# Optimization experiments

Measured on AMD Instinct MI355X. Metric: run time of the kernel, lower is better.

## Reference

```python
import jax, jax.numpy as jnp
import numpy as np

B, D_IN, D_COMMON = 16384, 2048, 1024
HIDDEN, D_OUT = 4096, 1024
N_EXPERTS = 4


def setup_inputs() -> dict:
    key = jax.random.key(0)
    ks = jax.random.split(key, 12)
    s = 0.02
    return {
        "x": jax.random.normal(ks[0], (B, D_IN), dtype=jnp.float32),
        "k": jax.random.randint(ks[1], (B,), 0, N_EXPERTS, dtype=jnp.int32),
        # per-key alignment Linear(D_IN -> D_COMMON), stored [in, out]
        "W_exp": jax.random.normal(ks[2], (N_EXPERTS, D_IN, D_COMMON), dtype=jnp.float32) * s,
        "b_exp": jax.random.normal(ks[3], (N_EXPERTS, D_COMMON), dtype=jnp.float32) * s,
        # dense MLP: common -> 4096 -> 4096 -> 1024
        "W1": jax.random.normal(ks[4], (D_COMMON, HIDDEN), dtype=jnp.float32) * s,
        "b1": jax.random.normal(ks[5], (HIDDEN,), dtype=jnp.float32) * s,
        "W2": jax.random.normal(ks[6], (HIDDEN, HIDDEN), dtype=jnp.float32) * s,
        "b2": jax.random.normal(ks[7], (HIDDEN,), dtype=jnp.float32) * s,
        "W3": jax.random.normal(ks[8], (HIDDEN, D_OUT), dtype=jnp.float32) * s,
        "b3": jax.random.normal(ks[9], (D_OUT,), dtype=jnp.float32) * s,
    }


def reference(x, k, W_exp, b_exp, W1, b1, W2, b2, W3, b3):
    # Key-routed per-row Linear: row i goes through expert k[i].
    # Compute all expert projections, then select per-row (vectorized dispatch).
    xW = jnp.einsum('bd,edc->ebc', x, W_exp)              # [E, B, common]
    onehot = jax.nn.one_hot(k, N_EXPERTS, dtype=x.dtype)  # [B, E]
    aligned = jnp.einsum('be,ebc->bc', onehot, xW) + b_exp[k]  # [B, common]
    # dense MLP with ReLU activations
    h = jax.nn.relu(aligned @ W1 + b1)
    h = jax.nn.relu(h @ W2 + b2)
    return h @ W3 + b3
```

## Files before the change

kernel.cpp:

```cpp
#include <hip/hip_runtime.h>
#include <stdint.h>

#define DEV static __device__ __forceinline__

typedef unsigned short u16;
typedef float  f32x4 __attribute__((ext_vector_type(4)));
typedef short  s16x8 __attribute__((ext_vector_type(8)));
typedef u16    u16x4 __attribute__((ext_vector_type(4)));

#define VMCNT(n) asm volatile("s_waitcnt vmcnt(" #n ")" ::: "memory")
#define BAR() __builtin_amdgcn_s_barrier()

DEV u16 f2bf(float f) {
  uint32_t u = __float_as_uint(f);
  u += 0x7FFFu + ((u >> 16) & 1u);
  return (u16)(u >> 16);
}

DEV void async16(const void* g, void* l) {
  __builtin_amdgcn_global_load_lds(
      (const __attribute__((address_space(1))) void*)g,
      (__attribute__((address_space(3))) void*)l, 16, 0, 0);
}

__global__ void route_zero(int* c) {
  if (threadIdx.x < 8) c[threadIdx.x] = 0;
}
__global__ void route_count(const int* __restrict__ k, int* __restrict__ c, int B) {
  int i = blockIdx.x * blockDim.x + threadIdx.x;
  if (i < B) atomicAdd(&c[k[i]], 1);
}
__global__ void route_scan(int* c) {
  if (threadIdx.x == 0) {
    int s = 0;
    for (int e = 0; e < 4; ++e) { c[8 + e] = s; s += c[e]; }
  }
}
__global__ void route_scatter(const int* __restrict__ k, int* __restrict__ c,
                              int* __restrict__ perm, int B) {
  int i = blockIdx.x * blockDim.x + threadIdx.x;
  if (i < B) {
    int e = k[i];
    int pos = atomicAdd(&c[4 + e], 1);
    perm[c[8 + e] + pos] = i;
  }
}

__global__ void cvt_f32_bf16(const float* __restrict__ src, u16* __restrict__ dst, long n4) {
  long i = (long)blockIdx.x * blockDim.x + threadIdx.x;
  long stride = (long)gridDim.x * blockDim.x;
  for (; i < n4; i += stride) {
    f32x4 v = ((const f32x4*)src)[i];
    u16x4 o;
    o.x = f2bf(v.x); o.y = f2bf(v.y); o.z = f2bf(v.z); o.w = f2bf(v.w);
    ((u16x4*)dst)[i] = o;
  }
}

__global__ void transpose_w(const float* __restrict__ src, u16* __restrict__ dst,
                            int R, int C) {
  __shared__ float t[32][33];
  long base = (long)blockIdx.z * R * C;
  int c0 = blockIdx.x * 32, r0 = blockIdx.y * 32;
  int tx = threadIdx.x, ty = threadIdx.y;
#pragma unroll
  for (int i = 0; i < 32; i += 8)
    t[ty + i][tx] = src[base + (long)(r0 + ty + i) * C + c0 + tx];
  __syncthreads();
#pragma unroll
  for (int i = 0; i < 32; i += 8)
    dst[base + (long)(c0 + ty + i) * R + r0 + tx] = f2bf(t[tx][ty + i]);
}


DEV void stageA(const u16* __restrict__ A, long K, long bm, int k0, int g,
                u16* lds, int tid) {
#pragma unroll
  for (int j = 0; j < 2; ++j) {
    int i = j * 512 + tid;
    int row = ((i >> 9) << 7) | (g << 6) | ((i >> 3) & 63);
    int p = (i & 7) * 16;
    int ke = (p ^ ((row & 7) << 4)) >> 1;
    async16(A + (bm + row) * K + k0 + ke, lds + row * 64 + (i & 7) * 8);
  }
}

DEV void stageB(const u16* __restrict__ Bt, long K, long bn, int k0, int g,
                u16* lds, int tid) {
#pragma unroll
  for (int j = 0; j < 2; ++j) {
    int i = j * 512 + tid;
    int col = ((i >> 8) << 6) | (g << 5) | ((i >> 3) & 31);
    int p = (i & 7) * 16;
    int ke = (p ^ ((col & 7) << 4)) >> 1;
    async16(Bt + (bn + col) * K + k0 + ke, lds + col * 64 + (i & 7) * 8);
  }
}

DEV void stageAg(const u16* __restrict__ X, long K, int k0, int g,
                 const long* ar, u16* lds, int tid) {
#pragma unroll
  for (int j = 0; j < 2; ++j) {
    int i = j * 512 + tid;
    int row = (j << 7) | (g << 6) | ((i >> 3) & 63);
    int p = (i & 7) * 16;
    int ke = (p ^ ((row & 7) << 4)) >> 1;
    async16(X + ar[j] * K + k0 + ke, lds + row * 64 + (i & 7) * 8);
  }
}

DEV s16x8 ldfrag(const u16* lds, int row, int ks, int lk) {
  int b = (ks * 64 + lk * 16) ^ ((row & 7) << 4);
  return *(const s16x8*)((const char*)(lds + row * 64) + b);
}

#define KT4(Ac, Bc, S1, S2, S3, S4)                                            \
  {                                                                            \
    _Pragma("unroll") for (int m = 0; m < 4; ++m)                              \
      _Pragma("unroll") for (int ks = 0; ks < 2; ++ks)                         \
        aa[m][ks] = ldfrag(Ac, wr * 128 + m * 16 + lr, ks, lk);                \
    _Pragma("unroll") for (int n = 0; n < 2; ++n)                              \
      _Pragma("unroll") for (int ks = 0; ks < 2; ++ks)                         \
        blo[n][ks] = ldfrag(Bc, wc * 64 + n * 16 + lr, ks, lk);                \
    S1;                                                                        \
    BAR();                                                                     \
    __builtin_amdgcn_s_setprio(1);                                             \
    _Pragma("unroll") for (int m = 0; m < 4; ++m)                              \
      _Pragma("unroll") for (int n = 0; n < 2; ++n)                            \
        _Pragma("unroll") for (int ks = 0; ks < 2; ++ks)                       \
          acc[m][n] = __builtin_amdgcn_mfma_f32_16x16x32_bf16(                 \
              aa[m][ks], blo[n][ks], acc[m][n], 0, 0, 0);                      \
    __builtin_amdgcn_s_setprio(0);                                             \
    _Pragma("unroll") for (int n = 0; n < 2; ++n)                              \
      _Pragma("unroll") for (int ks = 0; ks < 2; ++ks)                         \
        bhi[n][ks] = ldfrag(Bc, wc * 64 + (n + 2) * 16 + lr, ks, lk);          \
    S2;                                                                        \
    BAR();                                                                     \
    __builtin_amdgcn_s_setprio(1);                                             \
    _Pragma("unroll") for (int m = 0; m < 4; ++m)                              \
      _Pragma("unroll") for (int n = 0; n < 2; ++n)                            \
        _Pragma("unroll") for (int ks = 0; ks < 2; ++ks)                       \
          acc[m][n + 2] = __builtin_amdgcn_mfma_f32_16x16x32_bf16(             \
              aa[m][ks], bhi[n][ks], acc[m][n + 2], 0, 0, 0);                  \
    __builtin_amdgcn_s_setprio(0);                                             \
    _Pragma("unroll") for (int m = 0; m < 4; ++m)                              \
      _Pragma("unroll") for (int ks = 0; ks < 2; ++ks)                         \
        aa[m][ks] = ldfrag(Ac, wr * 128 + (m + 4) * 16 + lr, ks, lk);          \
    S3;                                                                        \
    BAR();                                                                     \
    __builtin_amdgcn_s_setprio(1);                                             \
    _Pragma("unroll") for (int m = 0; m < 4; ++m)                              \
      _Pragma("unroll") for (int n = 0; n < 2; ++n)                            \
        _Pragma("unroll") for (int ks = 0; ks < 2; ++ks)                       \
          acc[m + 4][n] = __builtin_amdgcn_mfma_f32_16x16x32_bf16(             \
              aa[m][ks], blo[n][ks], acc[m + 4][n], 0, 0, 0);                  \
    __builtin_amdgcn_s_setprio(0);                                             \
    S4;                                                                        \
    VMCNT(6);                                                                  \
    BAR();                                                                     \
    __builtin_amdgcn_s_setprio(1);                                             \
    _Pragma("unroll") for (int m = 0; m < 4; ++m)                              \
      _Pragma("unroll") for (int n = 0; n < 2; ++n)                            \
        _Pragma("unroll") for (int ks = 0; ks < 2; ++ks)                       \
          acc[m + 4][n + 2] = __builtin_amdgcn_mfma_f32_16x16x32_bf16(         \
              aa[m][ks], bhi[n][ks], acc[m + 4][n + 2], 0, 0, 0);              \
    __builtin_amdgcn_s_setprio(0);                                             \
  }

template <int RELU, int OUTF32>
__global__ __launch_bounds__(512, 2) void gemm256p(
    const u16* __restrict__ A, const u16* __restrict__ Bt,
    const float* __restrict__ bias, void* __restrict__ Cout, int N, int K) {
  __shared__ u16 Al[2][256 * 64];
  __shared__ u16 Bl[2][256 * 64];
  const int tid = threadIdx.x;
  const int lane = tid & 63, wid = tid >> 6;
  const int wr = wid >> 2, wc = wid & 3;
  const int lr = lane & 15, lk = lane >> 4;

  const int nby = N >> 8;
  const int nwg = gridDim.x;
  int wg = blockIdx.x;
  if ((nwg & 7) == 0) {
    const int q = nwg >> 3;
    wg = (wg & 7) * q + (wg >> 3);
  }
  const long bm = (long)(wg / nby) << 8;
  const long bn = (long)(wg % nby) << 8;

  const int nt = K >> 6;
  f32x4 acc[8][4] = {};
  s16x8 aa[4][2], blo[2][2], bhi[2][2];

  stageA(A, K, bm, 0, 0, Al[0], tid);
  stageB(Bt, K, bn, 0, 0, Bl[0], tid);
  stageB(Bt, K, bn, 0, 1, Bl[0], tid);
  stageA(A, K, bm, 0, 1, Al[0], tid);
  stageA(A, K, bm, 64, 0, Al[1], tid);
  stageB(Bt, K, bn, 64, 0, Bl[1], tid);
  stageB(Bt, K, bn, 64, 1, Bl[1], tid);
  VMCNT(6);
  BAR();

  const int ni = nt >> 1;
  for (int i2 = 0; i2 < ni; ++i2) {
    const int t0 = 2 * i2;
    const int kn1 = (t0 + 1) << 6;
    const int kn2 = ((t0 + 2 < nt) ? t0 + 2 : t0) << 6;
    const int kn3 = ((t0 + 3 < nt) ? t0 + 3 : t0 + 1) << 6;
    KT4(Al[0], Bl[0],
        stageA(A, K, bm, kn1, 1, Al[1], tid),
        stageA(A, K, bm, kn2, 0, Al[0], tid),
        stageB(Bt, K, bn, kn2, 0, Bl[0], tid),
        stageB(Bt, K, bn, kn2, 1, Bl[0], tid));
    KT4(Al[1], Bl[1],
        stageA(A, K, bm, kn2, 1, Al[0], tid),
        stageA(A, K, bm, kn3, 0, Al[1], tid),
        stageB(Bt, K, bn, kn3, 0, Bl[1], tid),
        stageB(Bt, K, bn, kn3, 1, Bl[1], tid));
  }

#pragma unroll
  for (int m = 0; m < 8; ++m) {
    const long r0 = bm + wr * 128 + m * 16 + lk * 4;
#pragma unroll
    for (int n = 0; n < 4; ++n) {
      const long col = bn + wc * 64 + n * 16 + lr;
      const float bv = bias[col];
#pragma unroll
      for (int j = 0; j < 4; ++j) {
        float v = acc[m][n][j] + bv;
        if (RELU) v = fmaxf(v, 0.0f);
        if (OUTF32) ((float*)Cout)[(r0 + j) * (long)N + col] = v;
        else        ((u16*)Cout)[(r0 + j) * (long)N + col] = f2bf(v);
      }
    }
  }
}

__global__ __launch_bounds__(512, 2) void gemm256e(
    const u16* __restrict__ X, const u16* __restrict__ Wt,
    const float* __restrict__ bexp, u16* __restrict__ Out,
    const int* __restrict__ perm, const int* __restrict__ cvec,
    int K, int N, int TPE) {
  __shared__ u16 Al[2][256 * 64];
  __shared__ u16 Bl[2][256 * 64];
  const int e = blockIdx.x / TPE;
  const int tile = blockIdx.x - e * TPE;
  const int cnt = cvec[e];
  if (tile * 256 >= cnt) return;
  const int start = cvec[8 + e];

  const int tid = threadIdx.x;
  const int lane = tid & 63, wid = tid >> 6;
  const int wr = wid >> 2, wc = wid & 3;
  const int lr = lane & 15, lk = lane >> 4;
  const long bn = (long)blockIdx.y << 8;
  const long wbase = (long)e * N;

  long ar[2][2];
#pragma unroll
  for (int g = 0; g < 2; ++g)
#pragma unroll
    for (int j = 0; j < 2; ++j) {
      int rie = tile * 256 + ((j << 7) | (g << 6) | ((tid >> 3) & 63));
      ar[g][j] = perm[start + (rie < cnt - 1 ? rie : cnt - 1)];
    }

  const int nt = K >> 6;
  f32x4 acc[8][4] = {};
  s16x8 aa[4][2], blo[2][2], bhi[2][2];

  stageAg(X, K, 0, 0, ar[0], Al[0], tid);
  stageB(Wt, K, wbase + bn, 0, 0, Bl[0], tid);
  stageB(Wt, K, wbase + bn, 0, 1, Bl[0], tid);
  stageAg(X, K, 0, 1, ar[1], Al[0], tid);
  stageAg(X, K, 64, 0, ar[0], Al[1], tid);
  stageB(Wt, K, wbase + bn, 64, 0, Bl[1], tid);
  stageB(Wt, K, wbase + bn, 64, 1, Bl[1], tid);
  VMCNT(6);
  BAR();

  const int ni = nt >> 1;
  for (int i2 = 0; i2 < ni; ++i2) {
    const int t0 = 2 * i2;
    const int kn1 = (t0 + 1) << 6;
    const int kn2 = ((t0 + 2 < nt) ? t0 + 2 : t0) << 6;
    const int kn3 = ((t0 + 3 < nt) ? t0 + 3 : t0 + 1) << 6;
    KT4(Al[0], Bl[0],
        stageAg(X, K, kn1, 1, ar[1], Al[1], tid),
        stageAg(X, K, kn2, 0, ar[0], Al[0], tid),
        stageB(Wt, K, wbase + bn, kn2, 0, Bl[0], tid),
        stageB(Wt, K, wbase + bn, kn2, 1, Bl[0], tid));
    KT4(Al[1], Bl[1],
        stageAg(X, K, kn2, 1, ar[1], Al[0], tid),
        stageAg(X, K, kn3, 0, ar[0], Al[1], tid),
        stageB(Wt, K, wbase + bn, kn3, 0, Bl[1], tid),
        stageB(Wt, K, wbase + bn, kn3, 1, Bl[1], tid));
  }

#pragma unroll
  for (int m = 0; m < 8; ++m) {
    const int rb = tile * 256 + wr * 128 + m * 16 + lk * 4;
#pragma unroll
    for (int j = 0; j < 4; ++j) {
      if (rb + j < cnt) {
        const long grow = perm[start + rb + j];
#pragma unroll
        for (int n = 0; n < 4; ++n) {
          const long col = bn + wc * 64 + n * 16 + lr;
          float v = acc[m][n][j] + bexp[wbase + col];
          Out[grow * (long)N + col] = f2bf(v);
        }
      }
    }
  }
}

extern "C" void kernel_launch(void* const* d_in, const int* in_sizes, int n_in,
                              void* d_out, int out_size, void* d_ws, size_t ws_size,
                              hipStream_t stream) {
  const float* x     = (const float*)d_in[0];
  const int*   kk    = (const int*)d_in[1];
  const float* W_exp = (const float*)d_in[2];
  const float* b_exp = (const float*)d_in[3];
  const float* W1    = (const float*)d_in[4];
  const float* b1    = (const float*)d_in[5];
  const float* W2    = (const float*)d_in[6];
  const float* b2    = (const float*)d_in[7];
  const float* W3    = (const float*)d_in[8];
  const float* b3    = (const float*)d_in[9];
  float* out = (float*)d_out;

  const int B = 16384, DIN = 2048, DC = 1024, H = 4096, DOUT = 1024, E = 4;

  uint8_t* ws = (uint8_t*)d_ws;
  const size_t MB = 1ull << 20;
  u16* xb    = (u16*)(ws + 0);
  u16* algn  = (u16*)(ws + 64 * MB);
  u16* h2    = (u16*)(ws + 0);
  u16* h1    = (u16*)(ws + 128 * MB);
  u16* wexpt = (u16*)(ws + 256 * MB);
  u16* w1t   = (u16*)(ws + 272 * MB);
  u16* w2t   = (u16*)(ws + 280 * MB);
  u16* w3t   = (u16*)(ws + 312 * MB);
  int* perm  = (int*)(ws + 320 * MB);
  int* cvec  = (int*)(ws + 320 * MB + 65536);

  route_zero<<<1, 64, 0, stream>>>(cvec);
  route_count<<<(B + 255) / 256, 256, 0, stream>>>(kk, cvec, B);
  route_scan<<<1, 64, 0, stream>>>(cvec);
  route_scatter<<<(B + 255) / 256, 256, 0, stream>>>(kk, cvec, perm, B);

  cvt_f32_bf16<<<2048, 256, 0, stream>>>(x, xb, (long)B * DIN / 4);
  dim3 tb(32, 8);
  transpose_w<<<dim3(DC / 32, DIN / 32, E), tb, 0, stream>>>(W_exp, wexpt, DIN, DC);
  transpose_w<<<dim3(H / 32, DC / 32, 1), tb, 0, stream>>>(W1, w1t, DC, H);
  transpose_w<<<dim3(H / 32, H / 32, 1), tb, 0, stream>>>(W2, w2t, H, H);
  transpose_w<<<dim3(DOUT / 32, H / 32, 1), tb, 0, stream>>>(W3, w3t, H, DOUT);

  const int TPE = B / 256;
  gemm256e<<<dim3(E * TPE, DC / 256), 512, 0, stream>>>(
      xb, wexpt, b_exp, algn, perm, cvec, DIN, DC, TPE);

  gemm256p<1, 0><<<dim3((B / 256) * (H / 256)), 512, 0, stream>>>(algn, w1t, b1, h1, H, DC);
  gemm256p<1, 0><<<dim3((B / 256) * (H / 256)), 512, 0, stream>>>(h1, w2t, b2, h2, H, H);
  gemm256p<0, 1><<<dim3((B / 256) * (DOUT / 256)), 512, 0, stream>>>(h2, w3t, b3, out, DOUT, H);
}
```

Baseline: 1.063 ms.

## Remap warps to 64x128 tiles and prefetch next-tile LDS fragments across barriers

Changes the per-warp tile from 128x64 (2x4 warp grid) to 64x128 (4x2 warp grid) in both the dense and expert-routed GEMM kernels. A fragments are now loaded once per K tile and reused across all four MFMA phases, while B fragments are streamed in four chunks, each read right after its barrier. The first A and B fragments for the next K tile are read from the other LDS buffer at the end of each phase, so those reads can overlap with the barrier and the staging of the following tile. The total LDS fragment reads stay the same; the aim is to shorten the exposed LDS latency before each MFMA block. The cost is that more fragments stay live in registers across barriers, which raises register pressure.

Measured after the change: 1.100 ms. 1.03x slower.

```diff
diff --git a/kernel.cpp b/kernel.cpp
--- a/kernel.cpp
+++ b/kernel.cpp
@@ -10,6 +10,7 @@
 
 #define VMCNT(n) asm volatile("s_waitcnt vmcnt(" #n ")" ::: "memory")
 #define BAR() __builtin_amdgcn_s_barrier()
+#define MFMA16(d, va, vb) d = __builtin_amdgcn_mfma_f32_16x16x32_bf16(va, vb, d, 0, 0, 0)
 
 DEV u16 f2bf(float f) {
   uint32_t u = __float_as_uint(f);
@@ -114,57 +115,60 @@
   return *(const s16x8*)((const char*)(lds + row * 64) + b);
 }
 
-#define KT4(Ac, Bc, S1, S2, S3, S4)                                            \
+#define KT4(Ac, Bc, An, Bn, S1, S2, S3, S4)                                    \
   {                                                                            \
-    _Pragma("unroll") for (int m = 0; m < 4; ++m)                              \
-      _Pragma("unroll") for (int ks = 0; ks < 2; ++ks)                         \
-        aa[m][ks] = ldfrag(Ac, wr * 128 + m * 16 + lr, ks, lk);                \
-    _Pragma("unroll") for (int n = 0; n < 2; ++n)                              \
-      _Pragma("unroll") for (int ks = 0; ks < 2; ++ks)                         \
-        blo[n][ks] = ldfrag(Bc, wc * 64 + n * 16 + lr, ks, lk);                \
+                    \
     S1;                                                                        \
     BAR();                                                                     \
+    _Pragma("unroll") for (int n = 0; n < 2; ++n)                              \
+      _Pragma("unroll") for (int ks = 0; ks < 2; ++ks)                         \
+        bB[n][ks] = ldfrag(Bc, wc * 128 + (n + 2) * 16 + lr, ks, lk);          \
     __builtin_amdgcn_s_setprio(1);                                             \
     _Pragma("unroll") for (int m = 0; m < 4; ++m)                              \
       _Pragma("unroll") for (int n = 0; n < 2; ++n)                            \
         _Pragma("unroll") for (int ks = 0; ks < 2; ++ks)                       \
-          acc[m][n] = __builtin_amdgcn_mfma_f32_16x16x32_bf16(                 \
-              aa[m][ks], blo[n][ks], acc[m][n], 0, 0, 0);                      \
+          MFMA16(acc[m][n], a[m][ks], bA[n][ks]);                              \
     __builtin_amdgcn_s_setprio(0);                                             \
-    _Pragma("unroll") for (int n = 0; n < 2; ++n)                              \
-      _Pragma("unroll") for (int ks = 0; ks < 2; ++ks)                         \
-        bhi[n][ks] = ldfrag(Bc, wc * 64 + (n + 2) * 16 + lr, ks, lk);          \
+                    \
     S2;                                                                        \
     BAR();                                                                     \
+    _Pragma("unroll") for (int n = 0; n < 2; ++n)                              \
+      _Pragma("unroll") for (int ks = 0; ks < 2; ++ks)                         \
+        bA[n][ks] = ldfrag(Bc, wc * 128 + (n + 4) * 16 + lr, ks, lk);          \
     __builtin_amdgcn_s_setprio(1);                                             \
     _Pragma("unroll") for (int m = 0; m < 4; ++m)                              \
       _Pragma("unroll") for (int n = 0; n < 2; ++n)                            \
         _Pragma("unroll") for (int ks = 0; ks < 2; ++ks)                       \
-          acc[m][n + 2] = __builtin_amdgcn_mfma_f32_16x16x32_bf16(             \
-              aa[m][ks], bhi[n][ks], acc[m][n + 2], 0, 0, 0);                  \
+          MFMA16(acc[m][n + 2], a[m][ks], bB[n][ks]);                          \
     __builtin_amdgcn_s_setprio(0);                                             \
-    _Pragma("unroll") for (int m = 0; m < 4; ++m)                              \
-      _Pragma("unroll") for (int ks = 0; ks < 2; ++ks)                         \
-        aa[m][ks] = ldfrag(Ac, wr * 128 + (m + 4) * 16 + lr, ks, lk);          \
+                    \
     S3;                                                                        \
     BAR();                                                                     \
+    _Pragma("unroll") for (int n = 0; n < 2; ++n)                              \
+      _Pragma("unroll") for (int ks = 0; ks < 2; ++ks)                         \
+        bB[n][ks] = ldfrag(Bc, wc * 128 + (n + 6) * 16 + lr, ks, lk);          \
     __builtin_amdgcn_s_setprio(1);                                             \
     _Pragma("unroll") for (int m = 0; m < 4; ++m)                              \
       _Pragma("unroll") for (int n = 0; n < 2; ++n)                            \
         _Pragma("unroll") for (int ks = 0; ks < 2; ++ks)                       \
-          acc[m + 4][n] = __builtin_amdgcn_mfma_f32_16x16x32_bf16(             \
-              aa[m][ks], blo[n][ks], acc[m + 4][n], 0, 0, 0);                  \
+          MFMA16(acc[m][n + 4], a[m][ks], bA[n][ks]);                          \
     __builtin_amdgcn_s_setprio(0);                                             \
+                   \
     S4;                                                                        \
     VMCNT(6);                                                                  \
     BAR();                                                                     \
+    _Pragma("unroll") for (int n = 0; n < 2; ++n)                              \
+      _Pragma("unroll") for (int ks = 0; ks < 2; ++ks)                         \
+        bA[n][ks] = ldfrag(Bn, wc * 128 + n * 16 + lr, ks, lk);                \
     __builtin_amdgcn_s_setprio(1);                                             \
     _Pragma("unroll") for (int m = 0; m < 4; ++m)                              \
       _Pragma("unroll") for (int n = 0; n < 2; ++n)                            \
         _Pragma("unroll") for (int ks = 0; ks < 2; ++ks)                       \
-          acc[m + 4][n + 2] = __builtin_amdgcn_mfma_f32_16x16x32_bf16(         \
-              aa[m][ks], bhi[n][ks], acc[m + 4][n + 2], 0, 0, 0);              \
+          MFMA16(acc[m][n + 6], a[m][ks], bB[n][ks]);                          \
     __builtin_amdgcn_s_setprio(0);                                             \
+    _Pragma("unroll") for (int m = 0; m < 4; ++m)                              \
+      _Pragma("unroll") for (int ks = 0; ks < 2; ++ks)                         \
+        a[m][ks] = ldfrag(An, wr * 64 + m * 16 + lr, ks, lk);                  \
   }
 
 template <int RELU, int OUTF32>
@@ -175,7 +179,7 @@
   __shared__ u16 Bl[2][256 * 64];
   const int tid = threadIdx.x;
   const int lane = tid & 63, wid = tid >> 6;
-  const int wr = wid >> 2, wc = wid & 3;
+  const int wr = wid >> 1, wc = wid & 1;
   const int lr = lane & 15, lk = lane >> 4;
 
   const int nby = N >> 8;
@@ -189,8 +193,8 @@
   const long bn = (long)(wg % nby) << 8;
 
   const int nt = K >> 6;
-  f32x4 acc[8][4] = {};
-  s16x8 aa[4][2], blo[2][2], bhi[2][2];
+  f32x4 acc[4][8] = {};
+  s16x8 a[4][2], bA[2][2], bB[2][2];
 
   stageA(A, K, bm, 0, 0, Al[0], tid);
   stageB(Bt, K, bn, 0, 0, Bl[0], tid);
@@ -202,18 +206,29 @@
   VMCNT(6);
   BAR();
 
+#pragma unroll
+  for (int m = 0; m < 4; ++m)
+#pragma unroll
+    for (int ks = 0; ks < 2; ++ks)
+      a[m][ks] = ldfrag(Al[0], wr * 64 + m * 16 + lr, ks, lk);
+#pragma unroll
+  for (int n = 0; n < 2; ++n)
+#pragma unroll
+    for (int ks = 0; ks < 2; ++ks)
+      bA[n][ks] = ldfrag(Bl[0], wc * 128 + n * 16 + lr, ks, lk);
+
   const int ni = nt >> 1;
   for (int i2 = 0; i2 < ni; ++i2) {
     const int t0 = 2 * i2;
     const int kn1 = (t0 + 1) << 6;
     const int kn2 = ((t0 + 2 < nt) ? t0 + 2 : t0) << 6;
     const int kn3 = ((t0 + 3 < nt) ? t0 + 3 : t0 + 1) << 6;
-    KT4(Al[0], Bl[0],
+    KT4(Al[0], Bl[0], Al[1], Bl[1],
         stageA(A, K, bm, kn1, 1, Al[1], tid),
         stageA(A, K, bm, kn2, 0, Al[0], tid),
         stageB(Bt, K, bn, kn2, 0, Bl[0], tid),
         stageB(Bt, K, bn, kn2, 1, Bl[0], tid));
-    KT4(Al[1], Bl[1],
+    KT4(Al[1], Bl[1], Al[0], Bl[0],
         stageA(A, K, bm, kn2, 1, Al[0], tid),
         stageA(A, K, bm, kn3, 0, Al[1], tid),
         stageB(Bt, K, bn, kn3, 0, Bl[1], tid),
@@ -221,11 +236,11 @@
   }
 
 #pragma unroll
-  for (int m = 0; m < 8; ++m) {
-    const long r0 = bm + wr * 128 + m * 16 + lk * 4;
-#pragma unroll
-    for (int n = 0; n < 4; ++n) {
-      const long col = bn + wc * 64 + n * 16 + lr;
+  for (int m = 0; m < 4; ++m) {
+    const long r0 = bm + wr * 64 + m * 16 + lk * 4;
+#pragma unroll
+    for (int n = 0; n < 8; ++n) {
+      const long col = bn + wc * 128 + n * 16 + lr;
       const float bv = bias[col];
 #pragma unroll
       for (int j = 0; j < 4; ++j) {
@@ -253,7 +268,7 @@
 
   const int tid = threadIdx.x;
   const int lane = tid & 63, wid = tid >> 6;
-  const int wr = wid >> 2, wc = wid & 3;
+  const int wr = wid >> 1, wc = wid & 1;
   const int lr = lane & 15, lk = lane >> 4;
   const long bn = (long)blockIdx.y << 8;
   const long wbase = (long)e * N;
@@ -268,8 +283,8 @@
     }
 
   const int nt = K >> 6;
-  f32x4 acc[8][4] = {};
-  s16x8 aa[4][2], blo[2][2], bhi[2][2];
+  f32x4 acc[4][8] = {};
+  s16x8 a[4][2], bA[2][2], bB[2][2];
 
   stageAg(X, K, 0, 0, ar[0], Al[0], tid);
   stageB(Wt, K, wbase + bn, 0, 0, Bl[0], tid);
@@ -281,18 +296,29 @@
   VMCNT(6);
   BAR();
 
+#pragma unroll
+  for (int m = 0; m < 4; ++m)
+#pragma unroll
+    for (int ks = 0; ks < 2; ++ks)
+      a[m][ks] = ldfrag(Al[0], wr * 64 + m * 16 + lr, ks, lk);
+#pragma unroll
+  for (int n = 0; n < 2; ++n)
+#pragma unroll
+    for (int ks = 0; ks < 2; ++ks)
+      bA[n][ks] = ldfrag(Bl[0], wc * 128 + n * 16 + lr, ks, lk);
+
   const int ni = nt >> 1;
   for (int i2 = 0; i2 < ni; ++i2) {
     const int t0 = 2 * i2;
     const int kn1 = (t0 + 1) << 6;
     const int kn2 = ((t0 + 2 < nt) ? t0 + 2 : t0) << 6;
     const int kn3 = ((t0 + 3 < nt) ? t0 + 3 : t0 + 1) << 6;
-    KT4(Al[0], Bl[0],
+    KT4(Al[0], Bl[0], Al[1], Bl[1],
         stageAg(X, K, kn1, 1, ar[1], Al[1], tid),
         stageAg(X, K, kn2, 0, ar[0], Al[0], tid),
         stageB(Wt, K, wbase + bn, kn2, 0, Bl[0], tid),
         stageB(Wt, K, wbase + bn, kn2, 1, Bl[0], tid));
-    KT4(Al[1], Bl[1],
+    KT4(Al[1], Bl[1], Al[0], Bl[0],
         stageAg(X, K, kn2, 1, ar[1], Al[0], tid),
         stageAg(X, K, kn3, 0, ar[0], Al[1], tid),
         stageB(Wt, K, wbase + bn, kn3, 0, Bl[1], tid),
@@ -300,15 +326,15 @@
   }
 
 #pragma unroll
-  for (int m = 0; m < 8; ++m) {
-    const int rb = tile * 256 + wr * 128 + m * 16 + lk * 4;
+  for (int m = 0; m < 4; ++m) {
+    const int rb = tile * 256 + wr * 64 + m * 16 + lk * 4;
 #pragma unroll
     for (int j = 0; j < 4; ++j) {
       if (rb + j < cnt) {
         const long grow = perm[start + rb + j];
 #pragma unroll
-        for (int n = 0; n < 4; ++n) {
-          const long col = bn + wc * 64 + n * 16 + lr;
+        for (int n = 0; n < 8; ++n) {
+          const long col = bn + wc * 128 + n * 16 + lr;
           float v = acc[m][n][j] + bexp[wbase + col];
           Out[grow * (long)N + col] = f2bf(v);
         }
```

## Replace dense MLP GEMMs with 128x256 tile, 4-wave, K=32 double-buffered kernel

Applied to the files above, without the earlier changes.

Swaps the 256x256-tile, 8-wave GEMM with a finely staged software pipeline for a new 128x256-tile kernel using 4 waves, a 32-wide K step, simple double buffering and a new LDS swizzle. Each wave now computes a 128x64 sub-tile, so every A fragment is shared across four N fragments. The smaller tile doubles the workgroup count and cuts LDS use per block, which may raise occupancy. In exchange it gives up the interleaved load/MFMA scheduling, waits on all outstanding loads every iteration, and rereads each weight tile twice as often overall.

After: 1.252 ms. +17.8%, slower.

```diff
diff --git a/kernel.cpp b/kernel.cpp
--- a/kernel.cpp
+++ b/kernel.cpp
@@ -10,6 +10,7 @@
 
 #define VMCNT(n) asm volatile("s_waitcnt vmcnt(" #n ")" ::: "memory")
 #define BAR() __builtin_amdgcn_s_barrier()
+#define MFMA16(d, va, vb) d = __builtin_amdgcn_mfma_f32_16x16x32_bf16(va, vb, d, 0, 0, 0)
 
 DEV u16 f2bf(float f) {
   uint32_t u = __float_as_uint(f);
@@ -73,15 +74,101 @@
 }
 
 
-DEV void stageA(const u16* __restrict__ A, long K, long bm, int k0, int g,
+DEV void stgA32(const u16* __restrict__ src, long K, long bm, int k0,
                 u16* lds, int tid) {
 #pragma unroll
   for (int j = 0; j < 2; ++j) {
-    int i = j * 512 + tid;
-    int row = ((i >> 9) << 7) | (g << 6) | ((i >> 3) & 63);
-    int p = (i & 7) * 16;
-    int ke = (p ^ ((row & 7) << 4)) >> 1;
-    async16(A + (bm + row) * K + k0 + ke, lds + row * 64 + (i & 7) * 8);
+    int i = j * 256 + tid;
+    int r = i >> 2;
+    int p = (i & 3) << 4;
+    int ke = (p ^ (((r >> 1) & 3) << 4)) >> 1;
+    async16(src + (bm + r) * K + k0 + ke, lds + i * 8);
+  }
+}
+
+DEV void stgB32(const u16* __restrict__ src, long K, long bn, int k0,
+                u16* lds, int tid) {
+#pragma unroll
+  for (int j = 0; j < 4; ++j) {
+    int i = j * 256 + tid;
+    int r = i >> 2;
+    int p = (i & 3) << 4;
+    int ke = (p ^ (((r >> 1) & 3) << 4)) >> 1;
+    async16(src + (bn + r) * K + k0 + ke, lds + i * 8);
+  }
+}
+
+DEV s16x8 ldfrag32(const u16* lds, int row, int lk) {
+  int b = (lk << 4) ^ (((row >> 1) & 3) << 4);
+  return *(const s16x8*)((const char*)lds + row * 64 + b);
+}
+
+template <int RELU, int OUTF32>
+__global__ __launch_bounds__(256, 2) void gemm128d(
+    const u16* __restrict__ A, const u16* __restrict__ Bt,
+    const float* __restrict__ bias, void* __restrict__ Cout, int N, int K) {
+  __shared__ u16 Al[2][128 * 32];
+  __shared__ u16 Bl[2][256 * 32];
+  const int tid = threadIdx.x;
+  const int lane = tid & 63;
+  const int wc = tid >> 6;
+  const int lr = lane & 15, lk = lane >> 4;
+
+  const int nby = N >> 8;
+  const int nwg = gridDim.x;
+  int wg = blockIdx.x;
+  if ((nwg & 7) == 0) {
+    const int q = nwg >> 3;
+    wg = (wg & 7) * q + (wg >> 3);
+  }
+  const long bm = (long)(wg / nby) << 7;
+  const long bn = (long)(wg % nby) << 8;
+
+  const int nt = K >> 5;
+  f32x4 acc[8][4] = {};
+
+  stgA32(A, K, bm, 0, Al[0], tid);
+  stgB32(Bt, K, bn, 0, Bl[0], tid);
+
+  for (int t = 0; t < nt; ++t) {
+    VMCNT(0);
+    BAR();
+    const int kn = ((t + 1 < nt) ? t + 1 : t) << 5;
+    stgA32(A, K, bm, kn, Al[(t + 1) & 1], tid);
+    stgB32(Bt, K, bn, kn, Bl[(t + 1) & 1], tid);
+    const u16* Ac = Al[t & 1];
+    const u16* Bc = Bl[t & 1];
+    s16x8 a[8], b[4];
+#pragma unroll
+    for (int m = 0; m < 8; ++m)
+      a[m] = ldfrag32(Ac, m * 16 + lr, lk);
+#pragma unroll
+    for (int n = 0; n < 4; ++n)
+      b[n] = ldfrag32(Bc, wc * 64 + n * 16 + lr, lk);
+    __builtin_amdgcn_s_setprio(1);
+#pragma unroll
+    for (int m = 0; m < 8; ++m)
+#pragma unroll
+      for (int n = 0; n < 4; ++n)
+        MFMA16(acc[m][n], a[m], b[n]);
+    __builtin_amdgcn_s_setprio(0);
+  }
+
+#pragma unroll
+  for (int m = 0; m < 8; ++m) {
+    const long r0 = bm + m * 16 + lk * 4;
+#pragma unroll
+    for (int n = 0; n < 4; ++n) {
+      const long col = bn + wc * 64 + n * 16 + lr;
+      const float bv = bias[col];
+#pragma unroll
+      for (int j = 0; j < 4; ++j) {
+        float v = acc[m][n][j] + bv;
+        if (RELU) v = fmaxf(v, 0.0f);
+        if (OUTF32) ((float*)Cout)[(r0 + j) * (long)N + col] = v;
+        else        ((u16*)Cout)[(r0 + j) * (long)N + col] = f2bf(v);
+      }
+    }
   }
 }
 
@@ -128,8 +215,7 @@
     _Pragma("unroll") for (int m = 0; m < 4; ++m)                              \
       _Pragma("unroll") for (int n = 0; n < 2; ++n)                            \
         _Pragma("unroll") for (int ks = 0; ks < 2; ++ks)                       \
-          acc[m][n] = __builtin_amdgcn_mfma_f32_16x16x32_bf16(                 \
-              aa[m][ks], blo[n][ks], acc[m][n], 0, 0, 0);                      \
+          MFMA16(acc[m][n], aa[m][ks], blo[n][ks]);                            \
     __builtin_amdgcn_s_setprio(0);                                             \
     _Pragma("unroll") for (int n = 0; n < 2; ++n)                              \
       _Pragma("unroll") for (int ks = 0; ks < 2; ++ks)                         \
@@ -140,8 +226,7 @@
     _Pragma("unroll") for (int m = 0; m < 4; ++m)                              \
       _Pragma("unroll") for (int n = 0; n < 2; ++n)                            \
         _Pragma("unroll") for (int ks = 0; ks < 2; ++ks)                       \
-          acc[m][n + 2] = __builtin_amdgcn_mfma_f32_16x16x32_bf16(             \
-              aa[m][ks], bhi[n][ks], acc[m][n + 2], 0, 0, 0);                  \
+          MFMA16(acc[m][n + 2], aa[m][ks], bhi[n][ks]);                        \
     __builtin_amdgcn_s_setprio(0);                                             \
     _Pragma("unroll") for (int m = 0; m < 4; ++m)                              \
       _Pragma("unroll") for (int ks = 0; ks < 2; ++ks)                         \
@@ -152,8 +237,7 @@
     _Pragma("unroll") for (int m = 0; m < 4; ++m)                              \
       _Pragma("unroll") for (int n = 0; n < 2; ++n)                            \
         _Pragma("unroll") for (int ks = 0; ks < 2; ++ks)                       \
-          acc[m + 4][n] = __builtin_amdgcn_mfma_f32_16x16x32_bf16(             \
-              aa[m][ks], blo[n][ks], acc[m + 4][n], 0, 0, 0);                  \
+          MFMA16(acc[m + 4][n], aa[m][ks], blo[n][ks]);                        \
     __builtin_amdgcn_s_setprio(0);                                             \
     S4;                                                                        \
     VMCNT(6);                                                                  \
@@ -162,81 +246,9 @@
     _Pragma("unroll") for (int m = 0; m < 4; ++m)                              \
       _Pragma("unroll") for (int n = 0; n < 2; ++n)                            \
         _Pragma("unroll") for (int ks = 0; ks < 2; ++ks)                       \
-          acc[m + 4][n + 2] = __builtin_amdgcn_mfma_f32_16x16x32_bf16(         \
-              aa[m][ks], bhi[n][ks], acc[m + 4][n + 2], 0, 0, 0);              \
+          MFMA16(acc[m + 4][n + 2], aa[m][ks], bhi[n][ks]);                    \
     __builtin_amdgcn_s_setprio(0);                                             \
   }
-
-template <int RELU, int OUTF32>
-__global__ __launch_bounds__(512, 2) void gemm256p(
-    const u16* __restrict__ A, const u16* __restrict__ Bt,
-    const float* __restrict__ bias, void* __restrict__ Cout, int N, int K) {
-  __shared__ u16 Al[2][256 * 64];
-  __shared__ u16 Bl[2][256 * 64];
-  const int tid = threadIdx.x;
-  const int lane = tid & 63, wid = tid >> 6;
-  const int wr = wid >> 2, wc = wid & 3;
-  const int lr = lane & 15, lk = lane >> 4;
-
-  const int nby = N >> 8;
-  const int nwg = gridDim.x;
-  int wg = blockIdx.x;
-  if ((nwg & 7) == 0) {
-    const int q = nwg >> 3;
-    wg = (wg & 7) * q + (wg >> 3);
-  }
-  const long bm = (long)(wg / nby) << 8;
-  const long bn = (long)(wg % nby) << 8;
-
-  const int nt = K >> 6;
-  f32x4 acc[8][4] = {};
-  s16x8 aa[4][2], blo[2][2], bhi[2][2];
-
-  stageA(A, K, bm, 0, 0, Al[0], tid);
-  stageB(Bt, K, bn, 0, 0, Bl[0], tid);
-  stageB(Bt, K, bn, 0, 1, Bl[0], tid);
-  stageA(A, K, bm, 0, 1, Al[0], tid);
-  stageA(A, K, bm, 64, 0, Al[1], tid);
-  stageB(Bt, K, bn, 64, 0, Bl[1], tid);
-  stageB(Bt, K, bn, 64, 1, Bl[1], tid);
-  VMCNT(6);
-  BAR();
-
-  const int ni = nt >> 1;
-  for (int i2 = 0; i2 < ni; ++i2) {
-    const int t0 = 2 * i2;
-    const int kn1 = (t0 + 1) << 6;
-    const int kn2 = ((t0 + 2 < nt) ? t0 + 2 : t0) << 6;
-    const int kn3 = ((t0 + 3 < nt) ? t0 + 3 : t0 + 1) << 6;
-    KT4(Al[0], Bl[0],
-        stageA(A, K, bm, kn1, 1, Al[1], tid),
-        stageA(A, K, bm, kn2, 0, Al[0], tid),
-        stageB(Bt, K, bn, kn2, 0, Bl[0], tid),
-        stageB(Bt, K, bn, kn2, 1, Bl[0], tid));
-    KT4(Al[1], Bl[1],
-        stageA(A, K, bm, kn2, 1, Al[0], tid),
-        stageA(A, K, bm, kn3, 0, Al[1], tid),
-        stageB(Bt, K, bn, kn3, 0, Bl[1], tid),
-        stageB(Bt, K, bn, kn3, 1, Bl[1], tid));
-  }
-
-#pragma unroll
-  for (int m = 0; m < 8; ++m) {
-    const long r0 = bm + wr * 128 + m * 16 + lk * 4;
-#pragma unroll
-    for (int n = 0; n < 4; ++n) {
-      const long col = bn + wc * 64 + n * 16 + lr;
-      const float bv = bias[col];
-#pragma unroll
-      for (int j = 0; j < 4; ++j) {
-        float v = acc[m][n][j] + bv;
-        if (RELU) v = fmaxf(v, 0.0f);
-        if (OUTF32) ((float*)Cout)[(r0 + j) * (long)N + col] = v;
-        else        ((u16*)Cout)[(r0 + j) * (long)N + col] = f2bf(v);
-      }
-    }
-  }
-}
 
 __global__ __launch_bounds__(512, 2) void gemm256e(
     const u16* __restrict__ X, const u16* __restrict__ Wt,
@@ -363,7 +375,7 @@
   gemm256e<<<dim3(E * TPE, DC / 256), 512, 0, stream>>>(
       xb, wexpt, b_exp, algn, perm, cvec, DIN, DC, TPE);
 
-  gemm256p<1, 0><<<dim3((B / 256) * (H / 256)), 512, 0, stream>>>(algn, w1t, b1, h1, H, DC);
-  gemm256p<1, 0><<<dim3((B / 256) * (H / 256)), 512, 0, stream>>>(h1, w2t, b2, h2, H, H);
-  gemm256p<0, 1><<<dim3((B / 256) * (DOUT / 256)), 512, 0, stream>>>(h2, w3t, b3, out, DOUT, H);
-}
+  gemm128d<1, 0><<<dim3((B / 128) * (H / 256)), 256, 0, stream>>>(algn, w1t, b1, h1, H, DC);
+  gemm128d<1, 0><<<dim3((B / 128) * (H / 256)), 256, 0, stream>>>(h1, w2t, b2, h2, H, H);
+  gemm128d<0, 1><<<dim3((B / 128) * (DOUT / 256)), 256, 0, stream>>>(h2, w3t, b3, out, DOUT, H);
+}
```
